# Optimization experiments

Hardware: AMD Instinct MI355X
Metric: run time of the kernel (lower is better)

Reference implementation:

```python
import jax, jax.numpy as jnp
import numpy as np

D_MODEL = 1024
N_HEAD = 16


def setup_inputs() -> dict:
    key = jax.random.key(0)
    ks = jax.random.split(key, 7)
    B, L, D = 2, 2048, D_MODEL
    s = 0.02
    return {
        "x": jax.random.normal(ks[0], (B, L, D), dtype=jnp.float32),
        "W_kq": jax.random.normal(ks[1], (D, 2 * D), dtype=jnp.float32) * s,
        "b_kq": jax.random.normal(ks[2], (2 * D,), dtype=jnp.float32) * s,
        "W_v": jax.random.normal(ks[3], (D, D), dtype=jnp.float32) * s,
        "b_v": jax.random.normal(ks[4], (D,), dtype=jnp.float32) * s,
        "W_o": jax.random.normal(ks[5], (D, D), dtype=jnp.float32) * s,
        "b_o": jax.random.normal(ks[6], (D,), dtype=jnp.float32) * s,
    }


def reference(x, W_kq, b_kq, W_v, b_v, W_o, b_o):
    B, L, D = x.shape
    H = N_HEAD
    dh = D // H
    kq = x @ W_kq + b_kq            # (B, L, 2D); split order: k first, then q
    k = kq[..., :D].reshape(B, L, H, dh)
    q = kq[..., D:].reshape(B, L, H, dh)
    v = (x @ W_v + b_v).reshape(B, L, H, dh)
    scale = 1.0 / jnp.sqrt(jnp.float32(dh))
    scores = jnp.einsum('blhd,bmhd->bhlm', q, k) * scale  # (B, H, L, L)
    causal = jnp.tril(jnp.ones((L, L), dtype=bool))
    scores = jnp.where(causal, scores, -jnp.inf)
    attn = jax.nn.softmax(scores, axis=-1)
    out = jnp.einsum('bhlm,bmhd->blhd', attn, v).reshape(B, L, D)
    out = out @ W_o + b_o
    return jnp.squeeze(out)
```

## Files before the change

kernel.cpp:

```cpp
#include <hip/hip_runtime.h>
#include <cstdint>


#define LSEQ 2048
#define DM   1024
#define BL   4096

using frag_ab = __attribute__((ext_vector_type(8))) short;
using half8   = __attribute__((ext_vector_type(8))) _Float16;
using half4   = __attribute__((ext_vector_type(4))) _Float16;
using half2_t = __attribute__((ext_vector_type(2))) _Float16;
using fp16x2  = __attribute__((ext_vector_type(2))) __fp16;
using f32x4   = __attribute__((ext_vector_type(4))) float;

__device__ __forceinline__ unsigned short f2bf(float f) {
  unsigned int u = __float_as_uint(f);
  u += 0x7fffu + ((u >> 16) & 1u);
  return (unsigned short)(u >> 16);
}

__device__ __forceinline__ half2_t pkrtz(float a, float b) {
  const fp16x2 r = __builtin_amdgcn_cvt_pkrtz(a, b);
  return __builtin_bit_cast(half2_t, r);
}

__device__ __forceinline__ void load_lds16(const void* g, void* l) {
  __builtin_amdgcn_global_load_lds(
      (const __attribute__((address_space(1))) unsigned int*)g,
      (__attribute__((address_space(3))) unsigned int*)l, 16, 0, 0);
}


__global__ __launch_bounds__(256) void prep_kernel(
    const float* __restrict__ x, unsigned short* __restrict__ xb,
    const float* __restrict__ W_kq, const float* __restrict__ W_v,
    const float* __restrict__ W_o,
    unsigned short* __restrict__ wcat, _Float16* __restrict__ wot)
{
  const int bid = blockIdx.x;
  const int tid = threadIdx.x;

  if (bid < 4096) {
    const int i = bid * 256 + tid;
    const float4 v = *(const float4*)&x[(size_t)i * 4];
    ushort4 o;
    o.x = f2bf(v.x); o.y = f2bf(v.y); o.z = f2bf(v.z); o.w = f2bf(v.w);
    *(ushort4*)&xb[(size_t)i * 4] = o;
    return;
  }

  __shared__ float tile[32][33];
  const int r  = tid >> 3;
  const int c4 = (tid & 7) * 4;

  const float* W;
  int N, nb, kb, which;
  if (bid < 6144) {
    const int b2 = bid - 4096;
    W = W_kq; N = 2048; nb = (b2 & 63) * 32; kb = (b2 >> 6) * 32; which = 0;
  } else if (bid < 7168) {
    const int b2 = bid - 6144;
    W = W_v;  N = 1024; nb = (b2 & 31) * 32; kb = (b2 >> 5) * 32; which = 1;
  } else {
    const int b2 = bid - 7168;
    W = W_o;  N = 1024; nb = (b2 & 31) * 32; kb = (b2 >> 5) * 32; which = 2;
  }

  const float4 v = *(const float4*)&W[(size_t)(kb + r) * N + nb + c4];
  tile[r][c4 + 0] = v.x; tile[r][c4 + 1] = v.y;
  tile[r][c4 + 2] = v.z; tile[r][c4 + 3] = v.w;
  __syncthreads();

  if (which == 2) {
    half4 o;
    o[0] = (_Float16)tile[c4 + 0][r];
    o[1] = (_Float16)tile[c4 + 1][r];
    o[2] = (_Float16)tile[c4 + 2][r];
    o[3] = (_Float16)tile[c4 + 3][r];
    *(half4*)&wot[(size_t)(nb + r) * 1024 + kb + c4] = o;
  } else {
    ushort4 o;
    o.x = f2bf(tile[c4 + 0][r]);
    o.y = f2bf(tile[c4 + 1][r]);
    o.z = f2bf(tile[c4 + 2][r]);
    o.w = f2bf(tile[c4 + 3][r]);
    unsigned short* dst = (which == 0) ? wcat : wcat + 2097152;
    *(ushort4*)&dst[(size_t)(nb + r) * 1024 + kb + c4] = o;
  }
}


__global__ __launch_bounds__(256, 3) void gemm_kqv(
    const unsigned short* __restrict__ A, const unsigned short* __restrict__ Bt,
    const float* __restrict__ b_kq, const float* __restrict__ b_v,
    unsigned short* __restrict__ kqb, _Float16* __restrict__ vtb)
{
  const int tid  = threadIdx.x;
  const int lane = tid & 63;
  const int w    = tid >> 6;
  const int wm   = (w >> 1) * 64;
  const int wn   = (w & 1) * 64;
  const int n0   = blockIdx.x * 128;
  const int m0   = blockIdx.y * 128;
  const int quad = lane >> 4;
  const int l15  = lane & 15;
  const int K    = 1024;

  __shared__ __align__(16) unsigned short As[128 * 64];
  __shared__ __align__(16) unsigned short Bs[128 * 64];

  const int srow = lane >> 3;
  const int sc   = (lane & 7) ^ srow;

  const unsigned short* gA = A  + (size_t)(m0 + w * 32 + srow) * K + sc * 8;
  const unsigned short* gB = Bt + (size_t)(n0 + w * 32 + srow) * K + sc * 8;

#define STAGE_AB(K0)                                                           \
  {                                                                            \
    _Pragma("unroll")                                                          \
    for (int i = 0; i < 4; ++i) {                                              \
      load_lds16(gA + (size_t)i * 8 * K + (K0),                                \
                 &As[(w * 32 + i * 8) * 64 + lane * 8]);                       \
      load_lds16(gB + (size_t)i * 8 * K + (K0),                                \
                 &Bs[(w * 32 + i * 8) * 64 + lane * 8]);                       \
    }                                                                          \
  }

  f32x4 acc[4][4] = {};

  STAGE_AB(0);
  asm volatile("s_waitcnt vmcnt(0)\n\ts_barrier" ::: "memory");

  for (int k0 = 0; k0 < K; k0 += 64) {
    frag_ab af[2][4], bf[2][4];
#pragma unroll
    for (int kf = 0; kf < 2; ++kf)
#pragma unroll
      for (int t = 0; t < 4; ++t) {
        const int ra = wm + t * 16 + l15;
        const int pa = (kf * 4 + quad) ^ (ra & 7);
        af[kf][t] = *(const frag_ab*)&As[ra * 64 + pa * 8];
        const int rb = wn + t * 16 + l15;
        const int pb = (kf * 4 + quad) ^ (rb & 7);
        bf[kf][t] = *(const frag_ab*)&Bs[rb * 64 + pb * 8];
      }
    asm volatile("s_waitcnt lgkmcnt(0)\n\ts_barrier" ::: "memory");
    if (k0 + 64 < K) STAGE_AB(k0 + 64);

    __builtin_amdgcn_s_setprio(1);
#pragma unroll
    for (int kf = 0; kf < 2; ++kf)
#pragma unroll
      for (int i = 0; i < 4; ++i)
#pragma unroll
        for (int j = 0; j < 4; ++j)
          acc[i][j] = __builtin_amdgcn_mfma_f32_16x16x32_bf16(
              af[kf][i], bf[kf][j], acc[i][j], 0, 0, 0);
    __builtin_amdgcn_s_setprio(0);

    asm volatile("s_waitcnt vmcnt(0)\n\ts_barrier" ::: "memory");
  }
#undef STAGE_AB

  if (n0 >= 2048) {
#pragma unroll
    for (int i = 0; i < 4; ++i)
#pragma unroll
      for (int j = 0; j < 4; ++j) {
        const int row0 = m0 + wm + i * 16 + quad * 4;
        const int col  = n0 - 2048 + wn + j * 16 + l15;
        const float bv = b_v[col];
        half4 pk;
        pk[0] = (_Float16)(acc[i][j][0] + bv);
        pk[1] = (_Float16)(acc[i][j][1] + bv);
        pk[2] = (_Float16)(acc[i][j][2] + bv);
        pk[3] = (_Float16)(acc[i][j][3] + bv);
        *(half4*)&vtb[(size_t)col * BL + row0] = pk;
      }
  } else {
    const float sc2 = (n0 + wn >= 1024) ? 0.18033688011112042f : 1.0f;
#pragma unroll
    for (int i = 0; i < 4; ++i)
#pragma unroll
      for (int j = 0; j < 4; ++j) {
        const int row0 = m0 + wm + i * 16 + quad * 4;
        const int col  = n0 + wn + j * 16 + l15;
        const float bv = b_kq[col];
#pragma unroll
        for (int r = 0; r < 4; ++r)
          kqb[(size_t)(row0 + r) * 2048 + col] = f2bf((acc[i][j][r] + bv) * sc2);
      }
  }
}


__global__ __launch_bounds__(256, 2) void gemm_out(
    const _Float16* __restrict__ A, const _Float16* __restrict__ Bt,
    const float* __restrict__ bias, float* __restrict__ C)
{
  const int tid  = threadIdx.x;
  const int lane = tid & 63;
  const int w    = tid >> 6;
  const int wm   = (w >> 1) * 64;
  const int wn   = (w & 1) * 32;
  const int n0   = blockIdx.x * 64;
  const int m0   = blockIdx.y * 128;
  const int quad = lane >> 4;
  const int l15  = lane & 15;
  const int K    = 1024;

  __shared__ __align__(16) _Float16 As[128 * 64];
  __shared__ __align__(16) _Float16 Bs[64 * 64];

  const int srow = lane >> 3;
  const int sc   = (lane & 7) ^ srow;

  const _Float16* gA = A  + (size_t)(m0 + w * 32 + srow) * K + sc * 8;
  const _Float16* gB = Bt + (size_t)(n0 + w * 16 + srow) * K + sc * 8;

#define STAGE_AB(K0)                                                           \
  {                                                                            \
    _Pragma("unroll")                                                          \
    for (int i = 0; i < 4; ++i)                                                \
      load_lds16(gA + (size_t)i * 8 * K + (K0),                                \
                 &As[(w * 32 + i * 8) * 64 + lane * 8]);                       \
    _Pragma("unroll")                                                          \
    for (int i = 0; i < 2; ++i)                                                \
      load_lds16(gB + (size_t)i * 8 * K + (K0),                                \
                 &Bs[(w * 16 + i * 8) * 64 + lane * 8]);                       \
  }

  f32x4 acc[4][2] = {};

  STAGE_AB(0);
  asm volatile("s_waitcnt vmcnt(0)\n\ts_barrier" ::: "memory");

  for (int k0 = 0; k0 < K; k0 += 64) {
    half8 af[2][4], bf[2][2];
#pragma unroll
    for (int kf = 0; kf < 2; ++kf) {
#pragma unroll
      for (int t = 0; t < 4; ++t) {
        const int ra = wm + t * 16 + l15;
        const int pa = (kf * 4 + quad) ^ (ra & 7);
        af[kf][t] = *(const half8*)&As[ra * 64 + pa * 8];
      }
#pragma unroll
      for (int t = 0; t < 2; ++t) {
        const int rb = wn + t * 16 + l15;
        const int pb = (kf * 4 + quad) ^ (rb & 7);
        bf[kf][t] = *(const half8*)&Bs[rb * 64 + pb * 8];
      }
    }
    asm volatile("s_waitcnt lgkmcnt(0)\n\ts_barrier" ::: "memory");
    if (k0 + 64 < K) STAGE_AB(k0 + 64);

    __builtin_amdgcn_s_setprio(1);
#pragma unroll
    for (int kf = 0; kf < 2; ++kf)
#pragma unroll
      for (int i = 0; i < 4; ++i)
#pragma unroll
        for (int j = 0; j < 2; ++j)
          acc[i][j] = __builtin_amdgcn_mfma_f32_16x16x32_f16(
              af[kf][i], bf[kf][j], acc[i][j], 0, 0, 0);
    __builtin_amdgcn_s_setprio(0);

    asm volatile("s_waitcnt vmcnt(0)\n\ts_barrier" ::: "memory");
  }
#undef STAGE_AB

#pragma unroll
  for (int i = 0; i < 4; ++i)
#pragma unroll
    for (int j = 0; j < 2; ++j) {
      const int row0 = m0 + wm + i * 16 + quad * 4;
      const int col  = n0 + wn + j * 16 + l15;
      const float bv = bias[col];
#pragma unroll
      for (int r = 0; r < 4; ++r)
        C[(size_t)(row0 + r) * DM + col] = acc[i][j][r] + bv;
    }
}


__global__ __launch_bounds__(256) void attn_mfma(
    const unsigned short* __restrict__ kq, const _Float16* __restrict__ vt,
    _Float16* __restrict__ att)
{
  const int tid  = threadIdx.x;
  const int lane = tid & 63;
  const int w    = tid >> 6;
  const int bx   = blockIdx.x;
  const int qt   = 31 - (bx >> 5);
  const int bh   = bx & 31;
  const int b    = bh >> 4;
  const int h    = bh & 15;
  const int q0   = qt * 64;
  const int quad = lane >> 4;
  const int l15  = lane & 15;

  __shared__ __align__(16) unsigned short Ks[128 * 64];
  __shared__ __align__(16) _Float16      Vs[64 * 128];

#pragma unroll
  for (int i = 0; i < 2; ++i) {
    const int L = i * 256 + tid;
    const int row = L >> 3, c = L & 7;
    const unsigned short* g = kq + (size_t)(b * LSEQ + q0 + row) * 2048
                                 + DM + h * 64 + ((c ^ (row & 7)) * 8);
    load_lds16(g, &Ks[(size_t)L * 8]);
  }
  asm volatile("s_waitcnt vmcnt(0)\n\ts_barrier" ::: "memory");
  frag_ab qa[2];
#pragma unroll
  for (int kf = 0; kf < 2; ++kf) {
    const int row = w * 16 + l15;
    const int c = (kf * 4 + quad) ^ (row & 7);
    qa[kf] = *(const frag_ab*)&Ks[row * 64 + c * 8];
  }
  asm volatile("s_waitcnt lgkmcnt(0)\n\ts_barrier" ::: "memory");

  const int nk = (qt + 2) >> 1;

#define STAGE_K(K0)                                                            \
  {                                                                            \
    _Pragma("unroll")                                                          \
    for (int i = 0; i < 4; ++i) {                                              \
      const int L = i * 256 + tid;                                             \
      const int row = L >> 3, c = L & 7;                                       \
      const unsigned short* g = kq + (size_t)(b * LSEQ + (K0) + row) * 2048    \
                                   + h * 64 + ((c ^ (row & 7)) * 8);           \
      load_lds16(g, &Ks[(size_t)L * 8]);                                       \
    }                                                                          \
  }
#define STAGE_V(K0)                                                            \
  {                                                                            \
    _Pragma("unroll")                                                          \
    for (int i = 0; i < 4; ++i) {                                              \
      const int L = i * 256 + tid;                                             \
      const int row = L >> 4, c16 = L & 15;                                    \
      const _Float16* g = vt + (size_t)(h * 64 + row) * BL                     \
                             + b * LSEQ + (K0) + ((c16 ^ (row & 15)) * 8);     \
      load_lds16(g, &Vs[(size_t)L * 8]);                                       \
    }                                                                          \
  }

  STAGE_K(0);
  STAGE_V(0);

  f32x4 oacc[4] = {};
  float mrow = -3e38f, lrow = 0.f;

  for (int kt = 0; kt < nk; ++kt) {
    const int k0 = kt * 128;
    const bool more = (kt + 1 < nk);

    asm volatile("s_waitcnt vmcnt(4)\n\ts_barrier" ::: "memory");

    f32x4 st[8];
    __builtin_amdgcn_s_setprio(1);
#pragma unroll
    for (int mt = 0; mt < 8; ++mt) {
      f32x4 s = {};
#pragma unroll
      for (int kf = 0; kf < 2; ++kf) {
        const int row = mt * 16 + l15;
        const int c = (kf * 4 + quad) ^ (row & 7);
        const frag_ab kfrag = *(const frag_ab*)&Ks[row * 64 + c * 8];
        s = __builtin_amdgcn_mfma_f32_16x16x32_bf16(kfrag, qa[kf], s, 0, 0, 0);
      }
      st[mt] = s;
    }
    __builtin_amdgcn_s_setprio(0);

    asm volatile("s_waitcnt lgkmcnt(0)\n\ts_barrier" ::: "memory");
    if (more) STAGE_K(k0 + 128);

    if (kt == nk - 1) {
      const int qg = q0 + w * 16 + l15;
#pragma unroll
      for (int mt = 0; mt < 8; ++mt)
#pragma unroll
        for (int r = 0; r < 4; ++r)
          if (k0 + mt * 16 + quad * 4 + r > qg) st[mt][r] = -3e38f;
    }

    float mx = fmaxf(st[0][0], st[0][1]);
    mx = fmaxf(fmaxf(mx, st[0][2]), st[0][3]);
#pragma unroll
    for (int mt = 1; mt < 8; ++mt) {
      mx = fmaxf(fmaxf(mx, st[mt][0]), st[mt][1]);
      mx = fmaxf(fmaxf(mx, st[mt][2]), st[mt][3]);
    }
    mx = fmaxf(mx, __shfl_xor(mx, 16));
    mx = fmaxf(mx, __shfl_xor(mx, 32));

    if (!__all(mx - mrow <= 8.0f)) {
      const float mnew  = fmaxf(mrow, mx);
      const float alpha = __builtin_amdgcn_exp2f(mrow - mnew);
      float aq[4];
#pragma unroll
      for (int r = 0; r < 4; ++r) aq[r] = __shfl(alpha, quad * 4 + r);
#pragma unroll
      for (int dt = 0; dt < 4; ++dt)
#pragma unroll
        for (int r = 0; r < 4; ++r) oacc[dt][r] *= aq[r];
      lrow *= alpha;
      mrow = mnew;
    }

    half4 pf[8];
    float rs0 = 0.f, rs1 = 0.f, rs2 = 0.f, rs3 = 0.f;
#pragma unroll
    for (int mt = 0; mt < 8; ++mt) {
      const float e0 = __builtin_amdgcn_exp2f(st[mt][0] - mrow);
      const float e1 = __builtin_amdgcn_exp2f(st[mt][1] - mrow);
      const float e2 = __builtin_amdgcn_exp2f(st[mt][2] - mrow);
      const float e3 = __builtin_amdgcn_exp2f(st[mt][3] - mrow);
      rs0 += e0; rs1 += e1; rs2 += e2; rs3 += e3;
      const half2_t p01 = pkrtz(e0, e1);
      const half2_t p23 = pkrtz(e2, e3);
      half4 p;
      p[0] = p01[0]; p[1] = p01[1]; p[2] = p23[0]; p[3] = p23[1];
      pf[mt] = p;
    }
    float rsum = (rs0 + rs1) + (rs2 + rs3);
    rsum += __shfl_xor(rsum, 16);
    rsum += __shfl_xor(rsum, 32);
    lrow += rsum;

    if (more) {
      asm volatile("s_waitcnt vmcnt(4)\n\ts_barrier" ::: "memory");
    } else {
      asm volatile("s_waitcnt vmcnt(0)\n\ts_barrier" ::: "memory");
    }

    __builtin_amdgcn_s_setprio(1);
#pragma unroll
    for (int c8 = 0; c8 < 8; ++c8) {
#pragma unroll
      for (int dt = 0; dt < 4; ++dt) {
        const int g16 = 2 * c8 + (quad >> 1);
        const half4 vf = *(const half4*)&Vs[(dt * 16 + l15) * 128
                                            + ((g16 ^ l15) << 3) + ((quad & 1) << 2)];
        oacc[dt] = __builtin_amdgcn_mfma_f32_16x16x16f16(pf[c8], vf, oacc[dt], 0, 0, 0);
      }
    }
    __builtin_amdgcn_s_setprio(0);

    if (more) {
      asm volatile("s_waitcnt lgkmcnt(0)\n\ts_barrier" ::: "memory");
      STAGE_V(k0 + 128);
    }
  }

  float lq[4];
#pragma unroll
  for (int r = 0; r < 4; ++r) lq[r] = 1.0f / __shfl(lrow, quad * 4 + r);
#pragma unroll
  for (int dt = 0; dt < 4; ++dt)
#pragma unroll
    for (int r = 0; r < 4; ++r) {
      const int row = b * LSEQ + q0 + w * 16 + quad * 4 + r;
      const int col = h * 64 + dt * 16 + l15;
      att[(size_t)row * DM + col] = (_Float16)(oacc[dt][r] * lq[r]);
    }
#undef STAGE_K
#undef STAGE_V
}


extern "C" void kernel_launch(void* const* d_in, const int* in_sizes, int n_in,
                              void* d_out, int out_size, void* d_ws, size_t ws_size,
                              hipStream_t stream)
{
  const float* x    = (const float*)d_in[0];
  const float* W_kq = (const float*)d_in[1];
  const float* b_kq = (const float*)d_in[2];
  const float* W_v  = (const float*)d_in[3];
  const float* b_v  = (const float*)d_in[4];
  const float* W_o  = (const float*)d_in[5];
  const float* b_o  = (const float*)d_in[6];

  unsigned short* ws   = (unsigned short*)d_ws;
  unsigned short* xb   = ws;
  unsigned short* wcat = xb   + 4194304;
  _Float16*       wot  = (_Float16*)(wcat + 3145728);
  unsigned short* kqb  = (unsigned short*)(wot + 1048576);
  _Float16*       vtb  = (_Float16*)(kqb + 8388608);
  _Float16*       attb = vtb + 4194304;

  prep_kernel<<<8192, 256, 0, stream>>>(x, xb, W_kq, W_v, W_o, wcat, wot);
  gemm_kqv<<<dim3(24, 32), 256, 0, stream>>>(xb, wcat, b_kq, b_v, kqb, vtb);
  attn_mfma<<<1024, 256, 0, stream>>>(kqb, vtb, attb);
  gemm_out<<<dim3(16, 32), 256, 0, stream>>>(attb, wot, b_o, (float*)d_out);
}
```

Before: 169.4 us.

## Process 128 query rows per attention block to reuse K/V tiles

Each attention block now handles a 128-row query tile, split into two 64-row halves A and B, instead of a 64-row tile, and the grid is halved to 512 blocks. Every K and V tile staged in shared memory feeds two sets of MFMAs and two online softmaxes, halving global K/V traffic per query row. In exchange, register pressure rises from duplicated accumulators, scores and probabilities, and fewer blocks with coarser causal work granularity may lower occupancy and worsen load balance. The first query half also does extra fully masked work on the diagonal tile.

Result: slower. 178.5 us (+5.4%).

```diff
diff --git a/kernel.cpp b/kernel.cpp
--- a/kernel.cpp
+++ b/kernel.cpp
@@ -292,11 +292,12 @@
   const int lane = tid & 63;
   const int w    = tid >> 6;
   const int bx   = blockIdx.x;
-  const int qt   = 31 - (bx >> 5);
+  const int t    = 15 - (bx >> 5);
   const int bh   = bx & 31;
   const int b    = bh >> 4;
   const int h    = bh & 15;
-  const int q0   = qt * 64;
+  const int q0   = t * 128;
+  const int nk   = t + 1;
   const int quad = lane >> 4;
   const int l15  = lane & 15;
 
@@ -304,7 +305,7 @@
   __shared__ __align__(16) _Float16      Vs[64 * 128];
 
 #pragma unroll
-  for (int i = 0; i < 2; ++i) {
+  for (int i = 0; i < 4; ++i) {
     const int L = i * 256 + tid;
     const int row = L >> 3, c = L & 7;
     const unsigned short* g = kq + (size_t)(b * LSEQ + q0 + row) * 2048
@@ -312,16 +313,17 @@
     load_lds16(g, &Ks[(size_t)L * 8]);
   }
   asm volatile("s_waitcnt vmcnt(0)\n\ts_barrier" ::: "memory");
-  frag_ab qa[2];
+  frag_ab qaA[2], qaB[2];
 #pragma unroll
   for (int kf = 0; kf < 2; ++kf) {
-    const int row = w * 16 + l15;
-    const int c = (kf * 4 + quad) ^ (row & 7);
-    qa[kf] = *(const frag_ab*)&Ks[row * 64 + c * 8];
+    const int rowA = w * 16 + l15;
+    const int cA = (kf * 4 + quad) ^ (rowA & 7);
+    qaA[kf] = *(const frag_ab*)&Ks[rowA * 64 + cA * 8];
+    const int rowB = 64 + w * 16 + l15;
+    const int cB = (kf * 4 + quad) ^ (rowB & 7);
+    qaB[kf] = *(const frag_ab*)&Ks[rowB * 64 + cB * 8];
   }
   asm volatile("s_waitcnt lgkmcnt(0)\n\ts_barrier" ::: "memory");
-
-  const int nk = (qt + 2) >> 1;
 
 #define STAGE_K(K0)                                                            \
   {                                                                            \
@@ -349,8 +351,8 @@
   STAGE_K(0);
   STAGE_V(0);
 
-  f32x4 oacc[4] = {};
-  float mrow = -3e38f, lrow = 0.f;
+  f32x4 oaccA[4] = {}, oaccB[4] = {};
+  float mrowA = -3e38f, lrowA = 0.f, mrowB = -3e38f, lrowB = 0.f;
 
   for (int kt = 0; kt < nk; ++kt) {
     const int k0 = kt * 128;
@@ -358,19 +360,20 @@
 
     asm volatile("s_waitcnt vmcnt(4)\n\ts_barrier" ::: "memory");
 
-    f32x4 st[8];
+    f32x4 stA[8], stB[8];
     __builtin_amdgcn_s_setprio(1);
 #pragma unroll
     for (int mt = 0; mt < 8; ++mt) {
-      f32x4 s = {};
+      f32x4 sA = {}, sB = {};
 #pragma unroll
       for (int kf = 0; kf < 2; ++kf) {
         const int row = mt * 16 + l15;
         const int c = (kf * 4 + quad) ^ (row & 7);
         const frag_ab kfrag = *(const frag_ab*)&Ks[row * 64 + c * 8];
-        s = __builtin_amdgcn_mfma_f32_16x16x32_bf16(kfrag, qa[kf], s, 0, 0, 0);
-      }
-      st[mt] = s;
+        sA = __builtin_amdgcn_mfma_f32_16x16x32_bf16(kfrag, qaA[kf], sA, 0, 0, 0);
+        sB = __builtin_amdgcn_mfma_f32_16x16x32_bf16(kfrag, qaB[kf], sB, 0, 0, 0);
+      }
+      stA[mt] = sA; stB[mt] = sB;
     }
     __builtin_amdgcn_s_setprio(0);
 
@@ -378,57 +381,66 @@
     if (more) STAGE_K(k0 + 128);
 
     if (kt == nk - 1) {
-      const int qg = q0 + w * 16 + l15;
+      const int qgA = q0 + w * 16 + l15;
+      const int qgB = qgA + 64;
 #pragma unroll
       for (int mt = 0; mt < 8; ++mt)
 #pragma unroll
-        for (int r = 0; r < 4; ++r)
-          if (k0 + mt * 16 + quad * 4 + r > qg) st[mt][r] = -3e38f;
-    }
-
-    float mx = fmaxf(st[0][0], st[0][1]);
-    mx = fmaxf(fmaxf(mx, st[0][2]), st[0][3]);
-#pragma unroll
-    for (int mt = 1; mt < 8; ++mt) {
-      mx = fmaxf(fmaxf(mx, st[mt][0]), st[mt][1]);
-      mx = fmaxf(fmaxf(mx, st[mt][2]), st[mt][3]);
-    }
-    mx = fmaxf(mx, __shfl_xor(mx, 16));
-    mx = fmaxf(mx, __shfl_xor(mx, 32));
-
-    if (!__all(mx - mrow <= 8.0f)) {
-      const float mnew  = fmaxf(mrow, mx);
-      const float alpha = __builtin_amdgcn_exp2f(mrow - mnew);
-      float aq[4];
-#pragma unroll
-      for (int r = 0; r < 4; ++r) aq[r] = __shfl(alpha, quad * 4 + r);
-#pragma unroll
-      for (int dt = 0; dt < 4; ++dt)
-#pragma unroll
-        for (int r = 0; r < 4; ++r) oacc[dt][r] *= aq[r];
-      lrow *= alpha;
-      mrow = mnew;
-    }
-
-    half4 pf[8];
-    float rs0 = 0.f, rs1 = 0.f, rs2 = 0.f, rs3 = 0.f;
-#pragma unroll
-    for (int mt = 0; mt < 8; ++mt) {
-      const float e0 = __builtin_amdgcn_exp2f(st[mt][0] - mrow);
-      const float e1 = __builtin_amdgcn_exp2f(st[mt][1] - mrow);
-      const float e2 = __builtin_amdgcn_exp2f(st[mt][2] - mrow);
-      const float e3 = __builtin_amdgcn_exp2f(st[mt][3] - mrow);
-      rs0 += e0; rs1 += e1; rs2 += e2; rs3 += e3;
-      const half2_t p01 = pkrtz(e0, e1);
-      const half2_t p23 = pkrtz(e2, e3);
-      half4 p;
-      p[0] = p01[0]; p[1] = p01[1]; p[2] = p23[0]; p[3] = p23[1];
-      pf[mt] = p;
-    }
-    float rsum = (rs0 + rs1) + (rs2 + rs3);
-    rsum += __shfl_xor(rsum, 16);
-    rsum += __shfl_xor(rsum, 32);
-    lrow += rsum;
+        for (int r = 0; r < 4; ++r) {
+          const int key = k0 + mt * 16 + quad * 4 + r;
+          if (key > qgA) stA[mt][r] = -3e38f;
+          if (key > qgB) stB[mt][r] = -3e38f;
+        }
+    }
+
+#define SOFTMAX(ST, MROW, LROW, PF, OACC)                                      \
+    {                                                                          \
+      float mx = fmaxf(ST[0][0], ST[0][1]);                                    \
+      mx = fmaxf(fmaxf(mx, ST[0][2]), ST[0][3]);                               \
+      _Pragma("unroll")                                                        \
+      for (int mt = 1; mt < 8; ++mt) {                                         \
+        mx = fmaxf(fmaxf(mx, ST[mt][0]), ST[mt][1]);                           \
+        mx = fmaxf(fmaxf(mx, ST[mt][2]), ST[mt][3]);                           \
+      }                                                                        \
+      mx = fmaxf(mx, __shfl_xor(mx, 16));                                      \
+      mx = fmaxf(mx, __shfl_xor(mx, 32));                                      \
+      if (!__all(mx - MROW <= 8.0f)) {                                         \
+        const float mnew  = fmaxf(MROW, mx);                                   \
+        const float alpha = __builtin_amdgcn_exp2f(MROW - mnew);               \
+        float aq[4];                                                           \
+        _Pragma("unroll")                                                      \
+        for (int r = 0; r < 4; ++r) aq[r] = __shfl(alpha, quad * 4 + r);       \
+        _Pragma("unroll")                                                      \
+        for (int dt = 0; dt < 4; ++dt)                                         \
+          _Pragma("unroll")                                                    \
+          for (int r = 0; r < 4; ++r) OACC[dt][r] *= aq[r];                    \
+        LROW *= alpha;                                                         \
+        MROW = mnew;                                                           \
+      }                                                                        \
+      float rs0 = 0.f, rs1 = 0.f, rs2 = 0.f, rs3 = 0.f;                        \
+      _Pragma("unroll")                                                        \
+      for (int mt = 0; mt < 8; ++mt) {                                         \
+        const float e0 = __builtin_amdgcn_exp2f(ST[mt][0] - MROW);             \
+        const float e1 = __builtin_amdgcn_exp2f(ST[mt][1] - MROW);             \
+        const float e2 = __builtin_amdgcn_exp2f(ST[mt][2] - MROW);             \
+        const float e3 = __builtin_amdgcn_exp2f(ST[mt][3] - MROW);             \
+        rs0 += e0; rs1 += e1; rs2 += e2; rs3 += e3;                            \
+        const half2_t p01 = pkrtz(e0, e1);                                     \
+        const half2_t p23 = pkrtz(e2, e3);                                     \
+        half4 p;                                                               \
+        p[0] = p01[0]; p[1] = p01[1]; p[2] = p23[0]; p[3] = p23[1];            \
+        PF[mt] = p;                                                            \
+      }                                                                        \
+      float rsum = (rs0 + rs1) + (rs2 + rs3);                                  \
+      rsum += __shfl_xor(rsum, 16);                                            \
+      rsum += __shfl_xor(rsum, 32);                                            \
+      LROW += rsum;                                                            \
+    }
+
+    half4 pfA[8], pfB[8];
+    SOFTMAX(stA, mrowA, lrowA, pfA, oaccA)
+    SOFTMAX(stB, mrowB, lrowB, pfB, oaccB)
+#undef SOFTMAX
 
     if (more) {
       asm volatile("s_waitcnt vmcnt(4)\n\ts_barrier" ::: "memory");
@@ -444,7 +456,8 @@
         const int g16 = 2 * c8 + (quad >> 1);
         const half4 vf = *(const half4*)&Vs[(dt * 16 + l15) * 128
                                             + ((g16 ^ l15) << 3) + ((quad & 1) << 2)];
-        oacc[dt] = __builtin_amdgcn_mfma_f32_16x16x16f16(pf[c8], vf, oacc[dt], 0, 0, 0);
+        oaccA[dt] = __builtin_amdgcn_mfma_f32_16x16x16f16(pfA[c8], vf, oaccA[dt], 0, 0, 0);
+        oaccB[dt] = __builtin_amdgcn_mfma_f32_16x16x16f16(pfB[c8], vf, oaccB[dt], 0, 0, 0);
       }
     }
     __builtin_amdgcn_s_setprio(0);
@@ -455,16 +468,20 @@
     }
   }
 
-  float lq[4];
-#pragma unroll
-  for (int r = 0; r < 4; ++r) lq[r] = 1.0f / __shfl(lrow, quad * 4 + r);
+  float lqA[4], lqB[4];
+#pragma unroll
+  for (int r = 0; r < 4; ++r) {
+    lqA[r] = 1.0f / __shfl(lrowA, quad * 4 + r);
+    lqB[r] = 1.0f / __shfl(lrowB, quad * 4 + r);
+  }
 #pragma unroll
   for (int dt = 0; dt < 4; ++dt)
 #pragma unroll
     for (int r = 0; r < 4; ++r) {
-      const int row = b * LSEQ + q0 + w * 16 + quad * 4 + r;
-      const int col = h * 64 + dt * 16 + l15;
-      att[(size_t)row * DM + col] = (_Float16)(oacc[dt][r] * lq[r]);
+      const int rowA = b * LSEQ + q0 + w * 16 + quad * 4 + r;
+      const int col  = h * 64 + dt * 16 + l15;
+      att[(size_t)rowA * DM + col] = (_Float16)(oaccA[dt][r] * lqA[r]);
+      att[(size_t)(rowA + 64) * DM + col] = (_Float16)(oaccB[dt][r] * lqB[r]);
     }
 #undef STAGE_K
 #undef STAGE_V
@@ -493,6 +510,6 @@
 
   prep_kernel<<<8192, 256, 0, stream>>>(x, xb, W_kq, W_v, W_o, wcat, wot);
   gemm_kqv<<<dim3(24, 32), 256, 0, stream>>>(xb, wcat, b_kq, b_v, kqb, vtb);
-  attn_mfma<<<1024, 256, 0, stream>>>(kqb, vtb, attb);
+  attn_mfma<<<512, 256, 0, stream>>>(kqb, vtb, attb);
   gemm_out<<<dim3(16, 32), 256, 0, stream>>>(attb, wot, b_o, (float*)d_out);
 }
```

## Double-buffer LDS tiles in output projection GEMM

Applied to the files above, without the earlier changes.

The output-projection GEMM now uses two LDS buffers, so the next K-tile is staged into one buffer while MFMAs read from the other. This leaves one barrier per K-step instead of two, and global-to-LDS loads can overlap the LDS reads and MFMA work. The cost is doubled LDS (48KB per block), which may limit the two blocks per CU that the launch bounds request.

Result: slower. 175.5 us (+3.6%).

```diff
diff --git a/kernel.cpp b/kernel.cpp
--- a/kernel.cpp
+++ b/kernel.cpp
@@ -209,8 +209,10 @@
   const int l15  = lane & 15;
   const int K    = 1024;
 
-  __shared__ __align__(16) _Float16 As[128 * 64];
-  __shared__ __align__(16) _Float16 Bs[64 * 64];
+  __shared__ __align__(16) _Float16 As0[128 * 64];
+  __shared__ __align__(16) _Float16 Bs0[64 * 64];
+  __shared__ __align__(16) _Float16 As1[128 * 64];
+  __shared__ __align__(16) _Float16 Bs1[64 * 64];
 
   const int srow = lane >> 3;
   const int sc   = (lane & 7) ^ srow;
@@ -218,57 +220,61 @@
   const _Float16* gA = A  + (size_t)(m0 + w * 32 + srow) * K + sc * 8;
   const _Float16* gB = Bt + (size_t)(n0 + w * 16 + srow) * K + sc * 8;
 
-#define STAGE_AB(K0)                                                           \
+#define STAGE_AB(K0, AS, BS)                                                   \
   {                                                                            \
     _Pragma("unroll")                                                          \
     for (int i = 0; i < 4; ++i)                                                \
       load_lds16(gA + (size_t)i * 8 * K + (K0),                                \
-                 &As[(w * 32 + i * 8) * 64 + lane * 8]);                       \
+                 &AS[(w * 32 + i * 8) * 64 + lane * 8]);                       \
     _Pragma("unroll")                                                          \
     for (int i = 0; i < 2; ++i)                                                \
       load_lds16(gB + (size_t)i * 8 * K + (K0),                                \
-                 &Bs[(w * 16 + i * 8) * 64 + lane * 8]);                       \
+                 &BS[(w * 16 + i * 8) * 64 + lane * 8]);                       \
+  }
+
+#define HALFSTEP(AS, BS, KNEXT, ASN, BSN)                                      \
+  {                                                                            \
+    asm volatile("s_waitcnt vmcnt(0)\n\ts_barrier" ::: "memory");              \
+    if ((KNEXT) < K) STAGE_AB((KNEXT), ASN, BSN);                              \
+    half8 af[2][4], bf[2][2];                                                  \
+    _Pragma("unroll")                                                          \
+    for (int kf = 0; kf < 2; ++kf) {                                           \
+      _Pragma("unroll")                                                        \
+      for (int t = 0; t < 4; ++t) {                                            \
+        const int ra = wm + t * 16 + l15;                                      \
+        const int pa = (kf * 4 + quad) ^ (ra & 7);                             \
+        af[kf][t] = *(const half8*)&AS[ra * 64 + pa * 8];                      \
+      }                                                                        \
+      _Pragma("unroll")                                                        \
+      for (int t = 0; t < 2; ++t) {                                            \
+        const int rb = wn + t * 16 + l15;                                      \
+        const int pb = (kf * 4 + quad) ^ (rb & 7);                             \
+        bf[kf][t] = *(const half8*)&BS[rb * 64 + pb * 8];                      \
+      }                                                                        \
+    }                                                                          \
+    __builtin_amdgcn_s_setprio(1);                                             \
+    _Pragma("unroll")                                                          \
+    for (int kf = 0; kf < 2; ++kf)                                             \
+      _Pragma("unroll")                                                        \
+      for (int i = 0; i < 4; ++i)                                              \
+        _Pragma("unroll")                                                      \
+        for (int j = 0; j < 2; ++j)                                            \
+          acc[i][j] = __builtin_amdgcn_mfma_f32_16x16x32_f16(                  \
+              af[kf][i], bf[kf][j], acc[i][j], 0, 0, 0);                       \
+    __builtin_amdgcn_s_setprio(0);                                             \
   }
 
   f32x4 acc[4][2] = {};
 
-  STAGE_AB(0);
-  asm volatile("s_waitcnt vmcnt(0)\n\ts_barrier" ::: "memory");
-
-  for (int k0 = 0; k0 < K; k0 += 64) {
-    half8 af[2][4], bf[2][2];
-#pragma unroll
-    for (int kf = 0; kf < 2; ++kf) {
-#pragma unroll
-      for (int t = 0; t < 4; ++t) {
-        const int ra = wm + t * 16 + l15;
-        const int pa = (kf * 4 + quad) ^ (ra & 7);
-        af[kf][t] = *(const half8*)&As[ra * 64 + pa * 8];
-      }
-#pragma unroll
-      for (int t = 0; t < 2; ++t) {
-        const int rb = wn + t * 16 + l15;
-        const int pb = (kf * 4 + quad) ^ (rb & 7);
-        bf[kf][t] = *(const half8*)&Bs[rb * 64 + pb * 8];
-      }
-    }
-    asm volatile("s_waitcnt lgkmcnt(0)\n\ts_barrier" ::: "memory");
-    if (k0 + 64 < K) STAGE_AB(k0 + 64);
-
-    __builtin_amdgcn_s_setprio(1);
-#pragma unroll
-    for (int kf = 0; kf < 2; ++kf)
-#pragma unroll
-      for (int i = 0; i < 4; ++i)
-#pragma unroll
-        for (int j = 0; j < 2; ++j)
-          acc[i][j] = __builtin_amdgcn_mfma_f32_16x16x32_f16(
-              af[kf][i], bf[kf][j], acc[i][j], 0, 0, 0);
-    __builtin_amdgcn_s_setprio(0);
-
-    asm volatile("s_waitcnt vmcnt(0)\n\ts_barrier" ::: "memory");
+  STAGE_AB(0, As0, Bs0);
+
+#pragma unroll 1
+  for (int k0 = 0; k0 < K; k0 += 128) {
+    HALFSTEP(As0, Bs0, k0 + 64, As1, Bs1)
+    HALFSTEP(As1, Bs1, k0 + 128, As0, Bs0)
   }
 #undef STAGE_AB
+#undef HALFSTEP
 
 #pragma unroll
   for (int i = 0; i < 4; ++i)
```
